# Kernel optimization log

Measured on AMD Instinct MI355X. Metric: run time of the kernel, lower is better.

## Reference

```python
import jax, jax.numpy as jnp
import numpy as np

FACTOR = 2  # upsample factor from init_kwargs


def _make_kernel_2d(kernel_1d):
    # outer product -> 2D separable FIR kernel, normalized to sum 1,
    # then scaled by factor**2 (gain compensation for zero-insertion upsampling)
    k = kernel_1d[None, :] * kernel_1d[:, None]
    k = k / jnp.sum(k)
    return k * (FACTOR ** 2)


def setup_inputs() -> dict:
    key = jax.random.key(0)
    k1, k2 = jax.random.split(key)
    x = jax.random.normal(k1, (8, 64, 256, 256), dtype=jnp.float32)
    # canonical StyleGAN FIR taps [1,3,3,1]
    kernel_1d = jnp.asarray([1.0, 3.0, 3.0, 1.0], dtype=jnp.float32)
    return {"x": x, "kernel_1d": kernel_1d}


def reference(x, kernel_1d):
    # upfirdn2d(x, k, up=factor, down=1, pad=(pad0, pad1))
    k2d = _make_kernel_2d(kernel_1d)            # [kh, kw]
    kh = k2d.shape[0]
    p = kh - FACTOR
    pad0 = (p + 1) // 2 + FACTOR - 1
    pad1 = p // 2

    # upfirdn uses true convolution (kernel flipped relative to correlation)
    kf = jnp.flip(k2d, (0, 1))
    C = x.shape[1]
    # depthwise filter, OIHW with I=1, same FIR taps for every channel
    w = jnp.broadcast_to(kf[None, None, :, :], (C, 1, kh, kh)).astype(x.dtype)

    # lhs_dilation fuses the zero-insertion upsample; padding fuses the pad step.
    # out spatial: FACTOR*(H-1)+1 + pad0 + pad1 - kh + 1 == FACTOR*H
    out = jax.lax.conv_general_dilated(
        x, w,
        window_strides=(1, 1),
        padding=((pad0, pad1), (pad0, pad1)),
        lhs_dilation=(FACTOR, FACTOR),
        dimension_numbers=("NCHW", "OIHW", "NCHW"),
        feature_group_count=C,
    )
    return out  # [B, C, FACTOR*H, FACTOR*W]
```

## Files before the change

kernel.cpp:

```cpp
#include <hip/hip_runtime.h>


#define IN_H 256
#define IN_W 256
#define OUT_H 511
#define OUT_W 511
#define N_BC (8 * 64)
#define STRIP 32
#define STRIPS (IN_H / STRIP)
#define CH 4
#define CHUNKS (STRIP / CH)
#define LDS_DW (8 * OUT_W + 8)

__global__ __launch_bounds__(256) void Upsample_64948495450678_kernel(
    const float* __restrict__ x,
    const float* __restrict__ k1d,
    float* __restrict__ out)
{
    __shared__ __align__(16) float lds[LDS_DW];

    const int t  = threadIdx.x;
    const int bc = blockIdx.x >> 3;
    const int r0 = (blockIdx.x & (STRIPS - 1)) * STRIP;

    const float k0 = k1d[0], k1 = k1d[1], k2 = k1d[2], k3 = k1d[3];
    const float inv = 2.0f / (k0 + k1 + k2 + k3);
    const float k0i = k0*inv, k1i = k1*inv, k2i = k2*inv, k3i = k3*inv;

    const int   p  = t & 1;
    const float wA = p ? k2i : k3i;
    const float wB = p ? k0i : k1i;
    const int   q0 = (t >> 1) + p;
    const int   q1 = q0 + 128;
    const bool  s1 = (t < 255);

    const float* __restrict__ xim = x + (size_t)bc * (IN_H * IN_W);

    float Hp0, Hp1;
    if (r0 == 0) {
        Hp0 = Hp1 = 0.0f;
    } else {
        const float* pr = xim + (size_t)(r0 - 1) * IN_W;
        const float a0 = (q0 > 0) ? pr[q0 - 1] : 0.0f;
        Hp0 = wA * a0 + wB * pr[q0];
        Hp1 = s1 ? (wA * pr[q1 - 1] + wB * pr[q1]) : 0.0f;
    }

    const size_t img_b = (size_t)bc * ((size_t)OUT_H * OUT_W * 4);
    char* __restrict__ outb = (char*)out;

    for (int c = 0; c < CHUNKS; ++c) {
        const int rc        = r0 + c * CH;
        const int row_start = (rc == 0) ? 0 : (2 * rc - 1);
        const int nrows     = (rc == 0) ? 7 : 8;
        const size_t S      = img_b + (size_t)row_start * (OUT_W * 4);
        const int pd        = (int)(S & 15) >> 2;

        for (int j = 0; j < CH; ++j) {
            const int r = rc + j;
            const float* pr = xim + (size_t)r * IN_W;
            const float a0 = (q0 > 0) ? pr[q0 - 1] : 0.0f;
            const float H0 = wA * a0 + wB * pr[q0];
            const float H1 = s1 ? (wA * pr[q1 - 1] + wB * pr[q1]) : 0.0f;

            if (r > 0) {
                float* L = lds + pd + (size_t)((2*r - 1) - row_start) * OUT_W;
                L[t] = k2i * Hp0 + k0i * H0;
                if (s1) L[t + 256] = k2i * Hp1 + k0i * H1;
            }
            {
                float* L = lds + pd + (size_t)(2*r - row_start) * OUT_W;
                L[t] = k3i * Hp0 + k1i * H0;
                if (s1) L[t + 256] = k3i * Hp1 + k1i * H1;
            }
            Hp0 = H0; Hp1 = H1;
        }
        __syncthreads();

        {
            const int nb     = nrows * (OUT_W * 4);
            const int headB  = (16 - (int)(S & 15)) & 15;
            const int nvec   = (nb - headB) >> 4;
            const int tailB  = (nb - headB) & 15;
            const int basedw = pd + (headB >> 2);
            char* gp = outb + S;

            if (t < (headB >> 2))
                *(float*)(gp + 4 * t) = lds[pd + t];

            for (int i = t; i < nvec; i += 256) {
                const float4 v = *(const float4*)(lds + basedw + 4 * i);
                *(float4*)(gp + headB + 16 * i) = v;
            }

            if (t < (tailB >> 2))
                *(float*)(gp + headB + 16 * nvec + 4 * t) =
                    lds[basedw + 4 * nvec + t];
        }
        __syncthreads();
    }
}

extern "C" void kernel_launch(void* const* d_in, const int* in_sizes, int n_in,
                              void* d_out, int out_size, void* d_ws, size_t ws_size,
                              hipStream_t stream) {
    const float* x   = (const float*)d_in[0];
    const float* k1d = (const float*)d_in[1];
    float* out = (float*)d_out;

    dim3 block(256, 1, 1);
    dim3 grid(N_BC * STRIPS, 1, 1);
    Upsample_64948495450678_kernel<<<grid, block, 0, stream>>>(x, k1d, out);
}
```

Measured before the change: 637.8 us.

## Give each wavefront its own row slice and LDS buffer, dropping block barriers

```diff
diff --git a/kernel.cpp b/kernel.cpp
--- a/kernel.cpp
+++ b/kernel.cpp
@@ -8,74 +8,84 @@
 #define N_BC (8 * 64)
 #define STRIP 32
 #define STRIPS (IN_H / STRIP)
-#define CH 4
-#define CHUNKS (STRIP / CH)
-#define LDS_DW (8 * OUT_W + 8)
+#define RPW (STRIP / 4)
+#define LDSW 1028
 
 __global__ __launch_bounds__(256) void Upsample_64948495450678_kernel(
     const float* __restrict__ x,
     const float* __restrict__ k1d,
     float* __restrict__ out)
 {
-    __shared__ __align__(16) float lds[LDS_DW];
+    __shared__ __align__(16) float lds[4 * LDSW];
 
     const int t  = threadIdx.x;
+    const int l  = t & 63;
+    const int w  = t >> 6;
     const int bc = blockIdx.x >> 3;
-    const int r0 = (blockIdx.x & (STRIPS - 1)) * STRIP;
+    const int rs = (blockIdx.x & (STRIPS - 1)) * STRIP + w * RPW;
+
+    float* __restrict__ L = lds + w * LDSW;
 
     const float k0 = k1d[0], k1 = k1d[1], k2 = k1d[2], k3 = k1d[3];
     const float inv = 2.0f / (k0 + k1 + k2 + k3);
     const float k0i = k0*inv, k1i = k1*inv, k2i = k2*inv, k3i = k3*inv;
 
-    const int   p  = t & 1;
-    const float wA = p ? k2i : k3i;
-    const float wB = p ? k0i : k1i;
-    const int   q0 = (t >> 1) + p;
-    const int   q1 = q0 + 128;
-    const bool  s1 = (t < 255);
-
     const float* __restrict__ xim = x + (size_t)bc * (IN_H * IN_W);
 
-    float Hp0, Hp1;
-    if (r0 == 0) {
-        Hp0 = Hp1 = 0.0f;
+    auto hrow = [&](const float4 v, float H[8]) {
+        const float um  = __shfl_up(v.w, 1);
+        const float xm1 = l ? um : 0.0f;
+        const float xp4 = __shfl_down(v.x, 1);
+        H[0] = k3i*xm1 + k1i*v.x;
+        H[1] = k2i*v.x + k0i*v.y;
+        H[2] = k3i*v.x + k1i*v.y;
+        H[3] = k2i*v.y + k0i*v.z;
+        H[4] = k3i*v.y + k1i*v.z;
+        H[5] = k2i*v.z + k0i*v.w;
+        H[6] = k3i*v.z + k1i*v.w;
+        H[7] = k2i*v.w + k0i*xp4;
+    };
+
+    float Hp[8];
+    if (rs == 0) {
+        #pragma unroll
+        for (int j = 0; j < 8; ++j) Hp[j] = 0.0f;
     } else {
-        const float* pr = xim + (size_t)(r0 - 1) * IN_W;
-        const float a0 = (q0 > 0) ? pr[q0 - 1] : 0.0f;
-        Hp0 = wA * a0 + wB * pr[q0];
-        Hp1 = s1 ? (wA * pr[q1 - 1] + wB * pr[q1]) : 0.0f;
+        const float4 vh = *(const float4*)(xim + (size_t)(rs - 1) * IN_W + 4 * l);
+        hrow(vh, Hp);
     }
+
+    float4 xc = *(const float4*)(xim + (size_t)rs * IN_W + 4 * l);
 
     const size_t img_b = (size_t)bc * ((size_t)OUT_H * OUT_W * 4);
     char* __restrict__ outb = (char*)out;
 
-    for (int c = 0; c < CHUNKS; ++c) {
-        const int rc        = r0 + c * CH;
-        const int row_start = (rc == 0) ? 0 : (2 * rc - 1);
-        const int nrows     = (rc == 0) ? 7 : 8;
+    for (int i = 0; i < RPW; ++i) {
+        const int r = rs + i;
+
+        float4 xn = xc;
+        if (i < RPW - 1)
+            xn = *(const float4*)(xim + (size_t)(r + 1) * IN_W + 4 * l);
+
+        float H[8];
+        hrow(xc, H);
+
+        const int row_start = r ? (2 * r - 1) : 0;
+        const int nrows     = r ? 2 : 1;
         const size_t S      = img_b + (size_t)row_start * (OUT_W * 4);
         const int pd        = (int)(S & 15) >> 2;
+        const int eoff      = r ? OUT_W : 0;
 
-        for (int j = 0; j < CH; ++j) {
-            const int r = rc + j;
-            const float* pr = xim + (size_t)r * IN_W;
-            const float a0 = (q0 > 0) ? pr[q0 - 1] : 0.0f;
-            const float H0 = wA * a0 + wB * pr[q0];
-            const float H1 = s1 ? (wA * pr[q1 - 1] + wB * pr[q1]) : 0.0f;
-
-            if (r > 0) {
-                float* L = lds + pd + (size_t)((2*r - 1) - row_start) * OUT_W;
-                L[t] = k2i * Hp0 + k0i * H0;
-                if (s1) L[t + 256] = k2i * Hp1 + k0i * H1;
+        if (r) {
+            #pragma unroll
+            for (int j = 0; j < 8; ++j) {
+                if (j < 7 || l < 63)
+                    L[pd + 8 * l + j] = k2i * Hp[j] + k0i * H[j];
             }
-            {
-                float* L = lds + pd + (size_t)(2*r - row_start) * OUT_W;
-                L[t] = k3i * Hp0 + k1i * H0;
-                if (s1) L[t + 256] = k3i * Hp1 + k1i * H1;
-            }
-            Hp0 = H0; Hp1 = H1;
         }
-        __syncthreads();
+        #pragma unroll
+        for (int j = 0; j < 8; ++j)
+            L[pd + eoff + 8 * l + j] = k3i * Hp[j] + k1i * H[j];
 
         {
             const int nb     = nrows * (OUT_W * 4);
@@ -85,19 +95,22 @@
             const int basedw = pd + (headB >> 2);
             char* gp = outb + S;
 
-            if (t < (headB >> 2))
-                *(float*)(gp + 4 * t) = lds[pd + t];
+            if (l < (headB >> 2))
+                *(float*)(gp + 4 * l) = L[pd + l];
 
-            for (int i = t; i < nvec; i += 256) {
-                const float4 v = *(const float4*)(lds + basedw + 4 * i);
-                *(float4*)(gp + headB + 16 * i) = v;
+            for (int v = l; v < nvec; v += 64) {
+                const float4 q = *(const float4*)(L + basedw + 4 * v);
+                *(float4*)(gp + headB + 16 * v) = q;
             }
 
-            if (t < (tailB >> 2))
-                *(float*)(gp + headB + 16 * nvec + 4 * t) =
-                    lds[basedw + 4 * nvec + t];
+            if (l < (tailB >> 2))
+                *(float*)(gp + headB + 16 * nvec + 4 * l) =
+                    L[basedw + 4 * nvec + l];
         }
-        __syncthreads();
+
+        #pragma unroll
+        for (int j = 0; j < 8; ++j) Hp[j] = H[j];
+        xc = xn;
     }
 }
 
```

Measured after the change: 648.7 us. No clear change (+1.7%).
